# Optimization experiments

Hardware: AMD Instinct MI355X
Metric: run time of the kernel (lower is better)

## Reference

```python
import jax, jax.numpy as jnp
import numpy as np


def _maxpool2x2(t):
    # t: [B, C, H, W] -> [B, C, H//2, W//2]
    B, C, H, W = t.shape
    return t.reshape(B, C, H // 2, 2, W // 2, 2).max(axis=(3, 5))


def setup_inputs() -> dict:
    key = jax.random.key(0)
    k_x, k_t, k_p, k_g, k_o = jax.random.split(key, 5)
    B, C, H, W = 16, 256, 64, 64
    C8, C2 = C // 8, C // 2
    scale = 1.0 / np.sqrt(C)
    return {
        "x": jax.random.normal(k_x, (B, C, H, W), dtype=jnp.float32),
        "w_theta": jax.random.normal(k_t, (C8, C), dtype=jnp.float32) * scale,
        "w_phi": jax.random.normal(k_p, (C8, C), dtype=jnp.float32) * scale,
        "w_g": jax.random.normal(k_g, (C2, C), dtype=jnp.float32) * scale,
        "w_o": jax.random.normal(k_o, (C, C2), dtype=jnp.float32) * (1.0 / np.sqrt(C2)),
        "gamma": jnp.ones((), dtype=jnp.float32),
    }


def reference(x, w_theta, w_phi, w_g, w_o, gamma):
    B, C, H, W = x.shape
    C8, C2 = C // 8, C // 2
    HW = H * W
    # 1x1 conv projections (pure channel GEMMs)
    theta = jnp.einsum("oc,bchw->bohw", w_theta, x)            # [B, C8, H, W]
    phi = _maxpool2x2(jnp.einsum("oc,bchw->bohw", w_phi, x))   # [B, C8, H/2, W/2]
    g = _maxpool2x2(jnp.einsum("oc,bchw->bohw", w_g, x))       # [B, C2, H/2, W/2]
    theta = theta.reshape(B, C8, HW)            # [B, C8, HW]
    phi = phi.reshape(B, C8, HW // 4)           # [B, C8, HW/4]
    g = g.reshape(B, C2, HW // 4)               # [B, C2, HW/4]
    # attention: no scaling, single head (BigGAN style)
    scores = jnp.einsum("bct,bcp->btp", theta, phi)   # [B, HW, HW/4]
    beta = jax.nn.softmax(scores, axis=-1)
    attn = jnp.einsum("bcp,btp->bct", g, beta)        # [B, C2, HW]
    attn = attn.reshape(B, C2, H, W)
    o = jnp.einsum("oc,bchw->bohw", w_o, attn)        # [B, C, H, W]
    return gamma * o + x
```

## Files before the change

### kernel.cpp

```cpp
#include <hip/hip_runtime.h>
#include <stdint.h>


#define B_  16
#define C_  256
#define HW_ 4096
#define C8_ 32
#define C2_ 128
#define P_  1024

#define WS_THETA 0u
#define WS_PHI   2097152u
#define WS_G     2621440u
#define WS_WOG   4718592u
#define WS_BETA  6815744u

__device__ inline unsigned short f2bf(float f) {
    unsigned int u = __builtin_bit_cast(unsigned int, f);
    u = (u + 0x7fffu + ((u >> 16) & 1u)) >> 16;
    return (unsigned short)u;
}
__device__ inline void beta_store4(unsigned short* p, float a, float b, float c, float d) {
    ushort4 v; v.x = f2bf(a); v.y = f2bf(b); v.z = f2bf(c); v.w = f2bf(d);
    *(ushort4*)p = v;
}
__device__ inline void splitbf(float f, unsigned short& h, unsigned short& l) {
    unsigned u = __builtin_bit_cast(unsigned, f);
    h = (unsigned short)(u >> 16);
    float lof = f - __builtin_bit_cast(float, u & 0xffff0000u);
    l = (unsigned short)(__builtin_bit_cast(unsigned, lof) >> 16);
}

typedef __attribute__((ext_vector_type(8))) short bf16x8;
typedef __attribute__((ext_vector_type(8))) unsigned short u16x8;
typedef __attribute__((ext_vector_type(4))) float f32x4;

#define GLOAD_LDS(gsrc, ldst) __builtin_amdgcn_global_load_lds( \
    (__attribute__((address_space(1))) void*)(uintptr_t)(const void*)(gsrc), \
    (__attribute__((address_space(3))) void*)(ldst), 16, 0, 0)

__global__ __launch_bounds__(256, 3) void k1_proj(
    const float* __restrict__ x, const float* __restrict__ w_theta,
    const float* __restrict__ w_phi, const float* __restrict__ w_g,
    float* __restrict__ theta_o, float* __restrict__ phi_o, float* __restrict__ g_o)
{
    const int ht = blockIdx.x, ogrp = blockIdx.y, b = blockIdx.z;
    const int tid = threadIdx.x;
    const int lane = tid & 63, wv = tid >> 6;
    const int lr = lane & 15, lk = lane >> 4;

    __shared__ float xs[64 * 128];
    __shared__ unsigned short WHs[64 * 72];
    __shared__ unsigned short WLs[64 * 72];

    const float* xb = x + ((size_t)b * C_) * HW_ + (size_t)ht * 128;
    const int c_ld = tid >> 2;
    const int sseg = (tid & 3) * 32;
    const int o_ld = tid >> 2;
    const int cseg = (tid & 3) * 16;

    const float* wsrc;
    if (ogrp == 0) wsrc = (o_ld < 32) ? (w_theta + o_ld * 256)
                                      : (w_phi + (o_ld - 32) * 256);
    else if (ogrp == 1) wsrc = w_g + o_ld * 256;
    else wsrc = w_g + (o_ld + 64) * 256;

    f32x4 acc[4][2] = {};

    for (int kc = 0; kc < 4; ++kc) {
        const int c0 = kc * 64;
        __syncthreads();
        {
            const float* src = xb + (size_t)(c0 + c_ld) * HW_ + sseg;
            #pragma unroll
            for (int u = 0; u < 8; ++u)
                *(float4*)&xs[c_ld * 128 + sseg + u * 4] = *(const float4*)&src[u * 4];
        }
        {
            #pragma unroll
            for (int h = 0; h < 2; ++h) {
                u16x8 hi, lo;
                #pragma unroll
                for (int e = 0; e < 8; ++e) {
                    unsigned short hh, ll;
                    splitbf(wsrc[c0 + cseg + h * 8 + e], hh, ll);
                    hi[e] = hh; lo[e] = ll;
                }
                *(u16x8*)&WHs[o_ld * 72 + cseg + h * 8] = hi;
                *(u16x8*)&WLs[o_ld * 72 + cseg + h * 8] = lo;
            }
        }
        __syncthreads();

        #pragma unroll
        for (int ks = 0; ks < 2; ++ks) {
            bf16x8 Ah[4], Al[4];
            #pragma unroll
            for (int mf = 0; mf < 4; ++mf) {
                Ah[mf] = *(const bf16x8*)&WHs[(mf * 16 + lr) * 72 + ks * 32 + lk * 8];
                Al[mf] = *(const bf16x8*)&WLs[(mf * 16 + lr) * 72 + ks * 32 + lk * 8];
            }
            #pragma unroll
            for (int nf = 0; nf < 2; ++nf) {
                const int s = wv * 32 + nf * 16 + lr;
                u16x8 hi, lo;
                #pragma unroll
                for (int e = 0; e < 8; ++e) {
                    unsigned short hh, ll;
                    splitbf(xs[(ks * 32 + lk * 8 + e) * 128 + s], hh, ll);
                    hi[e] = hh; lo[e] = ll;
                }
                const bf16x8 Bh = __builtin_bit_cast(bf16x8, hi);
                const bf16x8 Bl = __builtin_bit_cast(bf16x8, lo);
                #pragma unroll
                for (int mf = 0; mf < 4; ++mf) {
                    acc[mf][nf] = __builtin_amdgcn_mfma_f32_16x16x32_bf16(
                        Ah[mf], Bh, acc[mf][nf], 0, 0, 0);
                    acc[mf][nf] = __builtin_amdgcn_mfma_f32_16x16x32_bf16(
                        Ah[mf], Bl, acc[mf][nf], 0, 0, 0);
                    acc[mf][nf] = __builtin_amdgcn_mfma_f32_16x16x32_bf16(
                        Al[mf], Bh, acc[mf][nf], 0, 0, 0);
                }
            }
        }
    }

    __syncthreads();
    #pragma unroll
    for (int mf = 0; mf < 4; ++mf)
        #pragma unroll
        for (int nf = 0; nf < 2; ++nf)
            #pragma unroll
            for (int r = 0; r < 4; ++r)
                xs[(mf * 16 + lk * 4 + r) * 128 + wv * 32 + nf * 16 + lr]
                    = acc[mf][nf][r];
    __syncthreads();

    if (ogrp == 0) {
        {
            const int o = tid >> 3, k = (tid & 7) * 16;
            float* dst = theta_o + ((size_t)b * C8_ + o) * HW_ + (size_t)ht * 128 + k;
            #pragma unroll
            for (int u = 0; u < 4; ++u)
                *(float4*)&dst[u * 4] = *(float4*)&xs[o * 128 + k + u * 4];
        }
        {
            const int o2 = tid >> 3, wq = (tid & 7) * 4;
            float* dst = phi_o + ((size_t)b * C8_ + o2) * P_ + (size_t)ht * 32 + wq;
            #pragma unroll
            for (int u = 0; u < 4; ++u) {
                int w2 = wq + u;
                dst[u] = fmaxf(fmaxf(xs[(32 + o2) * 128 + 2 * w2],
                                     xs[(32 + o2) * 128 + 2 * w2 + 1]),
                               fmaxf(xs[(32 + o2) * 128 + 64 + 2 * w2],
                                     xs[(32 + o2) * 128 + 64 + 2 * w2 + 1]));
            }
        }
    } else {
        const int base = (ogrp - 1) * 64;
        const int o = tid >> 2, wq = (tid & 3) * 8;
        float* dst = g_o + ((size_t)b * C2_ + base + o) * P_ + (size_t)ht * 32 + wq;
        #pragma unroll
        for (int u = 0; u < 8; ++u) {
            int w2 = wq + u;
            dst[u] = fmaxf(fmaxf(xs[o * 128 + 2 * w2], xs[o * 128 + 2 * w2 + 1]),
                           fmaxf(xs[o * 128 + 64 + 2 * w2], xs[o * 128 + 64 + 2 * w2 + 1]));
        }
    }
}

__global__ __launch_bounds__(256) void k2_wog(
    const float* __restrict__ w_o, const float* __restrict__ g,
    unsigned short* __restrict__ wog)
{
    const int p0 = blockIdx.x * 64, cb = blockIdx.y, b = blockIdx.z;
    const int tid = threadIdx.x, wv = tid >> 6, lane = tid & 63;
    __shared__ float wls[64][128];
    __shared__ float gls[128][64];

    {
        const int o = tid >> 2, q = (tid & 3) * 32;
        const float* src = w_o + (size_t)(cb * 64 + o) * 128 + q;
        #pragma unroll
        for (int u = 0; u < 8; ++u)
            *(float4*)&wls[o][q + u * 4] = *(const float4*)&src[u * 4];
        const int c2 = tid >> 1, h = (tid & 1) * 32;
        const float* gsrc = g + ((size_t)b * C2_ + c2) * P_ + p0 + h;
        #pragma unroll
        for (int u = 0; u < 8; ++u)
            *(float4*)&gls[c2][h + u * 4] = *(const float4*)&gsrc[u * 4];
    }
    __syncthreads();

    float acc[16] = {};
    for (int k4 = 0; k4 < 32; ++k4) {
        float gk[4];
        #pragma unroll
        for (int kk = 0; kk < 4; ++kk) gk[kk] = gls[k4 * 4 + kk][lane];
        #pragma unroll
        for (int i = 0; i < 16; ++i) {
            float4 w4 = *(const float4*)&wls[wv * 16 + i][k4 * 4];
            acc[i] += w4.x * gk[0] + w4.y * gk[1] + w4.z * gk[2] + w4.w * gk[3];
        }
    }
    #pragma unroll
    for (int i = 0; i < 16; ++i)
        wog[((size_t)b * C_ + cb * 64 + wv * 16 + i) * P_ + p0 + lane] = f2bf(acc[i]);
}

__global__ __launch_bounds__(256) void k3_softmax(
    const float* __restrict__ theta, const float* __restrict__ phi,
    unsigned short* __restrict__ beta)
{
    const int t0 = blockIdx.x * 16, b = blockIdx.y;
    const int tid = threadIdx.x, wv = tid >> 6, lane = tid & 63;
    __shared__ float th[32][16];
    __shared__ float ph[32][256];

    if (tid < 128) {
        const int c = tid >> 2, tq = (tid & 3) * 4;
        *(float4*)&th[c][tq] =
            *(const float4*)&theta[((size_t)b * C8_ + c) * HW_ + t0 + tq];
    }

    float s[4][16] = {};
    #pragma unroll
    for (int ch = 0; ch < 4; ++ch) {
        __syncthreads();
        {
            const int c = tid >> 3, p8 = (tid & 7) * 4;
            const float* src = phi + ((size_t)b * C8_ + c) * P_ + ch * 256;
            #pragma unroll
            for (int u = 0; u < 8; ++u)
                *(float4*)&ph[c][p8 + u * 32] = *(const float4*)&src[p8 + u * 32];
        }
        __syncthreads();
        for (int c = 0; c < 32; ++c) {
            float4 pv = *(const float4*)&ph[c][lane * 4];
            #pragma unroll
            for (int r = 0; r < 4; ++r) {
                float tv = th[c][wv * 4 + r];
                s[r][ch * 4 + 0] += tv * pv.x;
                s[r][ch * 4 + 1] += tv * pv.y;
                s[r][ch * 4 + 2] += tv * pv.z;
                s[r][ch * 4 + 3] += tv * pv.w;
            }
        }
    }

    #pragma unroll
    for (int r = 0; r < 4; ++r) {
        float m = s[r][0];
        #pragma unroll
        for (int q = 1; q < 16; ++q) m = fmaxf(m, s[r][q]);
        #pragma unroll
        for (int off = 32; off > 0; off >>= 1) m = fmaxf(m, __shfl_xor(m, off));
        float sum = 0.f;
        #pragma unroll
        for (int q = 0; q < 16; ++q) { s[r][q] = __expf(s[r][q] - m); sum += s[r][q]; }
        #pragma unroll
        for (int off = 32; off > 0; off >>= 1) sum += __shfl_xor(sum, off);
        const float rl = 1.0f / sum;
        unsigned short* dst = beta + ((size_t)b * HW_ + t0 + wv * 4 + r) * P_;
        #pragma unroll
        for (int ch = 0; ch < 4; ++ch)
            beta_store4(&dst[ch * 256 + lane * 4],
                        s[r][ch * 4 + 0] * rl, s[r][ch * 4 + 1] * rl,
                        s[r][ch * 4 + 2] * rl, s[r][ch * 4 + 3] * rl);
    }
}

__global__ __launch_bounds__(256) void k4_mfma(
    const unsigned short* __restrict__ wog, const unsigned short* __restrict__ beta,
    const float* __restrict__ x, const float* __restrict__ gamma_p,
    float* __restrict__ out)
{
    const int t0 = blockIdx.x * 128, c0 = blockIdx.y * 128, b = blockIdx.z;
    const int tid = threadIdx.x, wv = tid >> 6, lane = tid & 63;
    const int wm = wv >> 1, wn = wv & 1;
    const int lr = lane & 15, lk = lane >> 4;
    __shared__ unsigned short As[128 * 64];
    __shared__ unsigned short Bs[128 * 64];

    f32x4 acc[4][4] = {};
    const unsigned short* wog_b  = wog  + ((size_t)b * C_  + c0) * P_;
    const unsigned short* beta_b = beta + ((size_t)b * HW_ + t0) * P_;

    for (int p0 = 0; p0 < 1024; p0 += 64) {
        __syncthreads();
        #pragma unroll
        for (int ch = 0; ch < 4; ++ch) {
            const int i16 = ch * 256 + tid;
            const int row = i16 >> 3, cb8 = i16 & 7;
            GLOAD_LDS(wog_b  + (size_t)row * P_ + p0 + cb8 * 8, &As[i16 * 8]);
            GLOAD_LDS(beta_b + (size_t)row * P_ + p0 + cb8 * 8, &Bs[i16 * 8]);
        }
        __syncthreads();

        #pragma unroll
        for (int ks = 0; ks < 2; ++ks) {
            bf16x8 af[4], bfr[4];
            #pragma unroll
            for (int mf = 0; mf < 4; ++mf)
                af[mf] = *(const bf16x8*)&As[(wm * 64 + mf * 16 + lr) * 64 + ks * 32 + lk * 8];
            #pragma unroll
            for (int nf = 0; nf < 4; ++nf)
                bfr[nf] = *(const bf16x8*)&Bs[(wn * 64 + nf * 16 + lr) * 64 + ks * 32 + lk * 8];
            #pragma unroll
            for (int mf = 0; mf < 4; ++mf)
                #pragma unroll
                for (int nf = 0; nf < 4; ++nf)
                    acc[mf][nf] = __builtin_amdgcn_mfma_f32_16x16x32_bf16(
                        af[mf], bfr[nf], acc[mf][nf], 0, 0, 0);
        }
    }

    const float gm = gamma_p[0];
    #pragma unroll
    for (int mf = 0; mf < 4; ++mf) {
        #pragma unroll
        for (int r = 0; r < 4; ++r) {
            const int co = c0 + wm * 64 + mf * 16 + lk * 4 + r;
            const size_t rowoff = ((size_t)b * C_ + co) * HW_;
            #pragma unroll
            for (int nf = 0; nf < 4; ++nf) {
                const int t = t0 + wn * 64 + nf * 16 + lr;
                out[rowoff + t] = gm * acc[mf][nf][r] + x[rowoff + t];
            }
        }
    }
}

extern "C" void kernel_launch(void* const* d_in, const int* in_sizes, int n_in,
                              void* d_out, int out_size, void* d_ws, size_t ws_size,
                              hipStream_t stream)
{
    const float* x       = (const float*)d_in[0];
    const float* w_theta = (const float*)d_in[1];
    const float* w_phi   = (const float*)d_in[2];
    const float* w_g     = (const float*)d_in[3];
    const float* w_o     = (const float*)d_in[4];
    const float* gamma   = (const float*)d_in[5];
    float* out = (float*)d_out;
    float* ws  = (float*)d_ws;

    float* theta          = ws + WS_THETA;
    float* phi            = ws + WS_PHI;
    float* g              = ws + WS_G;
    unsigned short* wog   = (unsigned short*)(ws + WS_WOG);
    unsigned short* beta  = (unsigned short*)(ws + WS_BETA);

    k1_proj<<<dim3(32, 3, 16), 256, 0, stream>>>(x, w_theta, w_phi, w_g,
                                                 theta, phi, g);
    k2_wog<<<dim3(16, 4, 16), 256, 0, stream>>>(w_o, g, wog);
    k3_softmax<<<dim3(256, 16), 256, 0, stream>>>(theta, phi, beta);
    k4_mfma<<<dim3(32, 2, 16), 256, 0, stream>>>(wog, beta, x, gamma, out);
}
```

Baseline: 332.0 us.

## Compute attention scores with split-bf16 MFMA using transposed theta/phi layouts

The score GEMM in the softmax kernel moves from scalar FP32 FMAs to bf16 MFMA instructions. Each operand is split into high and low bf16 parts and three MFMAs are combined to keep near-FP32 accuracy. The projection kernel now writes theta and phi transposed so the MFMA operands load contiguously. The softmax is redone across the MFMA output layout with shared-memory reductions between waves. The beta stores become scalar 2-byte writes, and the phi transpose store in k1 is strided.

```diff
diff --git a/kernel.cpp b/kernel.cpp
--- a/kernel.cpp
+++ b/kernel.cpp
@@ -42,7 +42,7 @@
 __global__ __launch_bounds__(256, 3) void k1_proj(
     const float* __restrict__ x, const float* __restrict__ w_theta,
     const float* __restrict__ w_phi, const float* __restrict__ w_g,
-    float* __restrict__ theta_o, float* __restrict__ phi_o, float* __restrict__ g_o)
+    float* __restrict__ thetaT_o, float* __restrict__ phiT_o, float* __restrict__ g_o)
 {
     const int ht = blockIdx.x, ogrp = blockIdx.y, b = blockIdx.z;
     const int tid = threadIdx.x;
@@ -138,22 +138,28 @@
 
     if (ogrp == 0) {
         {
-            const int o = tid >> 3, k = (tid & 7) * 16;
-            float* dst = theta_o + ((size_t)b * C8_ + o) * HW_ + (size_t)ht * 128 + k;
-            #pragma unroll
-            for (int u = 0; u < 4; ++u)
-                *(float4*)&dst[u * 4] = *(float4*)&xs[o * 128 + k + u * 4];
+            const int s = tid >> 1, o16 = (tid & 1) * 16;
+            float* dst = thetaT_o + ((size_t)b * HW_ + (size_t)ht * 128 + s) * 32 + o16;
+            #pragma unroll
+            for (int u = 0; u < 4; ++u) {
+                float4 v;
+                v.x = xs[(o16 + u * 4 + 0) * 128 + s];
+                v.y = xs[(o16 + u * 4 + 1) * 128 + s];
+                v.z = xs[(o16 + u * 4 + 2) * 128 + s];
+                v.w = xs[(o16 + u * 4 + 3) * 128 + s];
+                *(float4*)&dst[u * 4] = v;
+            }
         }
         {
             const int o2 = tid >> 3, wq = (tid & 7) * 4;
-            float* dst = phi_o + ((size_t)b * C8_ + o2) * P_ + (size_t)ht * 32 + wq;
             #pragma unroll
             for (int u = 0; u < 4; ++u) {
                 int w2 = wq + u;
-                dst[u] = fmaxf(fmaxf(xs[(32 + o2) * 128 + 2 * w2],
-                                     xs[(32 + o2) * 128 + 2 * w2 + 1]),
-                               fmaxf(xs[(32 + o2) * 128 + 64 + 2 * w2],
-                                     xs[(32 + o2) * 128 + 64 + 2 * w2 + 1]));
+                float pv = fmaxf(fmaxf(xs[(32 + o2) * 128 + 2 * w2],
+                                       xs[(32 + o2) * 128 + 2 * w2 + 1]),
+                                 fmaxf(xs[(32 + o2) * 128 + 64 + 2 * w2],
+                                       xs[(32 + o2) * 128 + 64 + 2 * w2 + 1]));
+                phiT_o[((size_t)b * P_ + (size_t)ht * 32 + w2) * 32 + o2] = pv;
             }
         }
     } else {
@@ -208,65 +214,129 @@
         wog[((size_t)b * C_ + cb * 64 + wv * 16 + i) * P_ + p0 + lane] = f2bf(acc[i]);
 }
 
-__global__ __launch_bounds__(256) void k3_softmax(
-    const float* __restrict__ theta, const float* __restrict__ phi,
+__global__ __launch_bounds__(256, 3) void k3_mfma(
+    const float* __restrict__ thetaT, const float* __restrict__ phiT,
     unsigned short* __restrict__ beta)
 {
     const int t0 = blockIdx.x * 16, b = blockIdx.y;
     const int tid = threadIdx.x, wv = tid >> 6, lane = tid & 63;
-    __shared__ float th[32][16];
-    __shared__ float ph[32][256];
+    const int lr = lane & 15, lk = lane >> 4;
+
+    __shared__ __align__(16) char sm[44032];
+    unsigned short* phH = (unsigned short*)sm;
+    unsigned short* phL = (unsigned short*)(sm + 20480);
+    unsigned short* thH = (unsigned short*)(sm + 40960);
+    unsigned short* thL = (unsigned short*)(sm + 42240);
+    float* red = (float*)(sm + 43520);
 
     if (tid < 128) {
-        const int c = tid >> 2, tq = (tid & 3) * 4;
-        *(float4*)&th[c][tq] =
-            *(const float4*)&theta[((size_t)b * C8_ + c) * HW_ + t0 + tq];
-    }
-
-    float s[4][16] = {};
+        const int t = tid >> 3, c4 = (tid & 7) * 4;
+        float4 v = *(const float4*)&thetaT[((size_t)b * HW_ + t0 + t) * 32 + c4];
+        ushort4 hv, lv;
+        splitbf(v.x, hv.x, lv.x); splitbf(v.y, hv.y, lv.y);
+        splitbf(v.z, hv.z, lv.z); splitbf(v.w, hv.w, lv.w);
+        *(ushort4*)&thH[t * 40 + c4] = hv;
+        *(ushort4*)&thL[t * 40 + c4] = lv;
+    }
+
+    f32x4 sc[16];
+
     #pragma unroll
     for (int ch = 0; ch < 4; ++ch) {
         __syncthreads();
         {
-            const int c = tid >> 3, p8 = (tid & 7) * 4;
-            const float* src = phi + ((size_t)b * C8_ + c) * P_ + ch * 256;
-            #pragma unroll
-            for (int u = 0; u < 8; ++u)
-                *(float4*)&ph[c][p8 + u * 32] = *(const float4*)&src[p8 + u * 32];
-        }
-        __syncthreads();
-        for (int c = 0; c < 32; ++c) {
-            float4 pv = *(const float4*)&ph[c][lane * 4];
-            #pragma unroll
-            for (int r = 0; r < 4; ++r) {
-                float tv = th[c][wv * 4 + r];
-                s[r][ch * 4 + 0] += tv * pv.x;
-                s[r][ch * 4 + 1] += tv * pv.y;
-                s[r][ch * 4 + 2] += tv * pv.z;
-                s[r][ch * 4 + 3] += tv * pv.w;
-            }
-        }
-    }
-
+            const float* src = &phiT[((size_t)b * P_ + ch * 256 + tid) * 32];
+            #pragma unroll
+            for (int g2 = 0; g2 < 4; ++g2) {
+                float4 a = *(const float4*)&src[g2 * 8];
+                float4 b4 = *(const float4*)&src[g2 * 8 + 4];
+                u16x8 hi, lo;
+                unsigned short hh, ll;
+                splitbf(a.x, hh, ll);  hi[0] = hh; lo[0] = ll;
+                splitbf(a.y, hh, ll);  hi[1] = hh; lo[1] = ll;
+                splitbf(a.z, hh, ll);  hi[2] = hh; lo[2] = ll;
+                splitbf(a.w, hh, ll);  hi[3] = hh; lo[3] = ll;
+                splitbf(b4.x, hh, ll); hi[4] = hh; lo[4] = ll;
+                splitbf(b4.y, hh, ll); hi[5] = hh; lo[5] = ll;
+                splitbf(b4.z, hh, ll); hi[6] = hh; lo[6] = ll;
+                splitbf(b4.w, hh, ll); hi[7] = hh; lo[7] = ll;
+                *(u16x8*)&phH[tid * 40 + g2 * 8] = hi;
+                *(u16x8*)&phL[tid * 40 + g2 * 8] = lo;
+            }
+        }
+        __syncthreads();
+
+        const bf16x8 Ah = *(const bf16x8*)&thH[lr * 40 + lk * 8];
+        const bf16x8 Al = *(const bf16x8*)&thL[lr * 40 + lk * 8];
+        #pragma unroll
+        for (int q = 0; q < 4; ++q) {
+            const int prow = wv * 64 + q * 16 + lr;
+            const bf16x8 Bh = *(const bf16x8*)&phH[prow * 40 + lk * 8];
+            const bf16x8 Bl = *(const bf16x8*)&phL[prow * 40 + lk * 8];
+            f32x4 a = {};
+            a = __builtin_amdgcn_mfma_f32_16x16x32_bf16(Ah, Bh, a, 0, 0, 0);
+            a = __builtin_amdgcn_mfma_f32_16x16x32_bf16(Ah, Bl, a, 0, 0, 0);
+            a = __builtin_amdgcn_mfma_f32_16x16x32_bf16(Al, Bh, a, 0, 0, 0);
+            sc[ch * 4 + q] = a;
+        }
+    }
+
+    float mrow[4], rl[4];
     #pragma unroll
     for (int r = 0; r < 4; ++r) {
-        float m = s[r][0];
-        #pragma unroll
-        for (int q = 1; q < 16; ++q) m = fmaxf(m, s[r][q]);
-        #pragma unroll
-        for (int off = 32; off > 0; off >>= 1) m = fmaxf(m, __shfl_xor(m, off));
-        float sum = 0.f;
-        #pragma unroll
-        for (int q = 0; q < 16; ++q) { s[r][q] = __expf(s[r][q] - m); sum += s[r][q]; }
-        #pragma unroll
-        for (int off = 32; off > 0; off >>= 1) sum += __shfl_xor(sum, off);
-        const float rl = 1.0f / sum;
-        unsigned short* dst = beta + ((size_t)b * HW_ + t0 + wv * 4 + r) * P_;
-        #pragma unroll
-        for (int ch = 0; ch < 4; ++ch)
-            beta_store4(&dst[ch * 256 + lane * 4],
-                        s[r][ch * 4 + 0] * rl, s[r][ch * 4 + 1] * rl,
-                        s[r][ch * 4 + 2] * rl, s[r][ch * 4 + 3] * rl);
+        float m = sc[0][r];
+        #pragma unroll
+        for (int qg = 1; qg < 16; ++qg) m = fmaxf(m, sc[qg][r]);
+        #pragma unroll
+        for (int off = 1; off < 16; off <<= 1) m = fmaxf(m, __shfl_xor(m, off));
+        mrow[r] = m;
+    }
+    __syncthreads();
+    if (lr == 0) {
+        #pragma unroll
+        for (int r = 0; r < 4; ++r) red[(lk * 4 + r) * 4 + wv] = mrow[r];
+    }
+    __syncthreads();
+    #pragma unroll
+    for (int r = 0; r < 4; ++r) {
+        const int t = lk * 4 + r;
+        mrow[r] = fmaxf(fmaxf(red[t * 4 + 0], red[t * 4 + 1]),
+                        fmaxf(red[t * 4 + 2], red[t * 4 + 3]));
+    }
+    __syncthreads();
+
+    float ssum[4];
+    #pragma unroll
+    for (int r = 0; r < 4; ++r) {
+        float s = 0.f;
+        #pragma unroll
+        for (int qg = 0; qg < 16; ++qg) {
+            float e = __expf(sc[qg][r] - mrow[r]);
+            sc[qg][r] = e; s += e;
+        }
+        #pragma unroll
+        for (int off = 1; off < 16; off <<= 1) s += __shfl_xor(s, off);
+        ssum[r] = s;
+    }
+    if (lr == 0) {
+        #pragma unroll
+        for (int r = 0; r < 4; ++r) red[(lk * 4 + r) * 4 + wv] = ssum[r];
+    }
+    __syncthreads();
+    #pragma unroll
+    for (int r = 0; r < 4; ++r) {
+        const int t = lk * 4 + r;
+        rl[r] = 1.0f / (red[t * 4 + 0] + red[t * 4 + 1] +
+                        red[t * 4 + 2] + red[t * 4 + 3]);
+    }
+
+    unsigned short* bb = beta + ((size_t)b * HW_ + t0) * P_;
+    #pragma unroll
+    for (int qg = 0; qg < 16; ++qg) {
+        const int p = (qg >> 2) * 256 + wv * 64 + (qg & 3) * 16 + lr;
+        #pragma unroll
+        for (int r = 0; r < 4; ++r)
+            bb[(size_t)(lk * 4 + r) * P_ + p] = f2bf(sc[qg][r] * rl[r]);
     }
 }
 
@@ -344,15 +414,15 @@
     float* out = (float*)d_out;
     float* ws  = (float*)d_ws;
 
-    float* theta          = ws + WS_THETA;
-    float* phi            = ws + WS_PHI;
+    float* thetaT         = ws + WS_THETA;
+    float* phiT           = ws + WS_PHI;
     float* g              = ws + WS_G;
     unsigned short* wog   = (unsigned short*)(ws + WS_WOG);
     unsigned short* beta  = (unsigned short*)(ws + WS_BETA);
 
     k1_proj<<<dim3(32, 3, 16), 256, 0, stream>>>(x, w_theta, w_phi, w_g,
-                                                 theta, phi, g);
+                                                 thetaT, phiT, g);
     k2_wog<<<dim3(16, 4, 16), 256, 0, stream>>>(w_o, g, wog);
-    k3_softmax<<<dim3(256, 16), 256, 0, stream>>>(theta, phi, beta);
+    k3_mfma<<<dim3(256, 16), 256, 0, stream>>>(thetaT, phiT, beta);
     k4_mfma<<<dim3(32, 2, 16), 256, 0, stream>>>(wog, beta, x, gamma, out);
 }
```

After: 321.0 us. -3.3%, faster.
